# Kernel tuning notes

Hardware: AMD Instinct MI355X
Metric: run time of the kernel (lower is better)

Reference implementation:

```python
import jax, jax.numpy as jnp
import numpy as np
from jax import lax

V, E, H = 32000, 512, 512
B, K, S, T = 16, 8, 50, 40
SOS, EOS, UNK, PAD = 2, 3, 0, 1
MIN_LEN, DD, NEG = 3, 0.1, -1e20
N = B * K


def setup_inputs():
    key = jax.random.key(0)
    ks = jax.random.split(key, 12)
    w = lambda k, sh: jax.random.normal(k, sh, dtype=jnp.float32) * 0.05
    return {
        "src": jax.random.randint(ks[0], (S, B), 4, V, dtype=jnp.int32),
        "src_len": jax.random.randint(ks[1], (B,), 5, S + 1, dtype=jnp.int32),
        "embed": w(ks[2], (V, E)),
        "enc_Wih": w(ks[3], (3 * H, E)), "enc_Whh": w(ks[4], (3 * H, H)),
        "enc_bih": jnp.zeros((3 * H,), jnp.float32), "enc_bhh": jnp.zeros((3 * H,), jnp.float32),
        "bridge_W": w(ks[5], (H, H)), "bridge_b": jnp.zeros((H,), jnp.float32),
        "dec_Wih": w(ks[6], (3 * H, E)), "dec_Whh": w(ks[7], (3 * H, H)),
        "dec_bih": jnp.zeros((3 * H,), jnp.float32), "dec_bhh": jnp.zeros((3 * H,), jnp.float32),
        "attn_W": w(ks[8], (H, H)),
        "comb_W": w(ks[9], (H, 2 * H)), "comb_b": jnp.zeros((H,), jnp.float32),
        "out_W": w(ks[10], (V, H)), "out_b": jnp.zeros((V,), jnp.float32),
    }


def _gru_cell(x, h, Wih, Whh, bih, bhh):
    # torch nn.GRU cell math
    gi = x @ Wih.T + bih
    gh = h @ Whh.T + bhh
    ir, iz, inn = jnp.split(gi, 3, axis=-1)
    hr, hz, hn = jnp.split(gh, 3, axis=-1)
    r = jax.nn.sigmoid(ir + hr)
    z = jax.nn.sigmoid(iz + hz)
    n = jnp.tanh(inn + r * hn)
    return (1.0 - z) * n + z * h


def _beam_search(src, src_len, embed, enc_Wih, enc_Whh, enc_bih, enc_bhh,
                 bridge_W, bridge_b, dec_Wih, dec_Whh, dec_bih, dec_bhh,
                 attn_W, comb_W, comb_b, out_W, out_b):
    # ---- encoder: uni-dir GRU with length masking ----
    def enc_step(h, xt):
        x_t, t = xt
        hn = _gru_cell(embed[x_t], h, enc_Wih, enc_Whh, enc_bih, enc_bhh)
        h = jnp.where((t < src_len)[:, None], hn, h)
        return h, h

    h_fin, enc_outs = lax.scan(enc_step, jnp.zeros((B, H), embed.dtype), (src, jnp.arange(S)))
    hidden = jnp.tanh(h_fin @ bridge_W.T + bridge_b)  # LinearBridge

    # ---- beam expansion (repeat_interleave over batch dim) ----
    enc_bank = jnp.repeat(enc_outs, K, axis=1).transpose(1, 0, 2)  # [N,S,H]
    src_len_b = jnp.repeat(src_len, K)                              # [N]
    hidden = jnp.repeat(hidden, K, axis=0)                          # [N,H]
    attn_mask = jnp.arange(S)[None, :] < src_len_b[:, None]         # [N,S]

    def dec_step(tok, h):
        h = _gru_cell(embed[tok], h, dec_Wih, dec_Whh, dec_bih, dec_bhh)
        sc = jnp.einsum('nh,nsh->ns', h @ attn_W.T, enc_bank)
        a = jax.nn.softmax(jnp.where(attn_mask, sc, -1e9), axis=-1)
        ctx = jnp.einsum('ns,nsh->nh', a, enc_bank)
        o = jnp.tanh(jnp.concatenate([h, ctx], axis=-1) @ comb_W.T + comb_b)
        return jax.nn.log_softmax(o @ out_W.T + out_b, axis=-1), h

    padding_logits = jnp.full((B, K, K), NEG, jnp.float32).at[:, :, 0].set(0.0)
    dd_off = jnp.broadcast_to(-(jnp.arange(K, dtype=jnp.float32) * DD), (B, K, K))
    flat_offsets = jnp.repeat(jnp.arange(0, N, K), K)  # [N]

    last_token = jnp.full((N,), SOS, jnp.int32)
    tokens = jnp.zeros((T, N), jnp.int32).at[0].set(last_token)
    ending = jnp.zeros((N,), bool)
    dec_len = jnp.zeros((N,), jnp.float32)
    beam_scores = jnp.zeros((T, B, K), jnp.float32).at[0].set(
        jnp.full((B, K), NEG, jnp.float32).at[:, 0].set(0.0))

    def step(carry, t):
        last_token, hidden, ending, dec_len, beam_scores, tokens = carry
        logp, hidden = dec_step(last_token, hidden)
        logp = logp.at[:, EOS].set(jnp.where(t <= MIN_LEN, NEG, logp[:, EOS]))
        logp = logp.at[:, UNK].set(NEG)  # disable_unk_output
        p = logp.reshape(B, K, V)
        tk_sc, tk_idx = lax.top_k(p, K)                       # [B,K,K]
        tk_sc = tk_sc + jnp.where(t > 1, 1.0, 0.0) * dd_off   # diverse decoding
        endf = ending.reshape(B, K, 1)
        fin = jnp.where(endf, -tk_sc + padding_logits, 0.0)   # finished-beam offsets
        total = beam_scores.sum(axis=0)                        # [B,K]
        tot = (tk_sc + total[:, :, None] + fin).reshape(B, K * K)
        cur = (tk_sc + fin).reshape(B, K * K)
        tmp_len = jnp.where(ending, dec_len, dec_len + 1.0)
        grp_tok = tk_idx.reshape(B, K * K)
        _, sel = lax.top_k(tot, K)                             # [B,K]
        sel_tok = jnp.take_along_axis(grp_tok, sel, axis=1)
        cur_sc = jnp.take_along_axis(cur, sel, axis=1)
        flat_idx = (sel // K).reshape(-1) + flat_offsets
        hidden = hidden[flat_offsets]  # faithful: source uses flatten_offsets here
        beam_scores = beam_scores.reshape(T, N)[:, flat_idx].reshape(T, B, K)
        tokens = tokens[:, flat_idx]
        ending = ending[flat_idx]
        dec_len = tmp_len[flat_idx]
        last_token = jnp.where(ending, PAD, sel_tok.reshape(-1)).astype(jnp.int32)
        tokens = tokens.at[t].set(last_token)
        beam_scores = beam_scores.at[t].set(
            cur_sc * (last_token.reshape(B, K) != PAD).astype(jnp.float32))
        ending = ending | (last_token == EOS)
        return (last_token, hidden, ending, dec_len, beam_scores, tokens), None

    carry = (last_token, hidden, ending, dec_len, beam_scores, tokens)
    (_, _, _, _, beam_scores, tokens), _ = lax.scan(step, carry, jnp.arange(1, T))
    return tokens, beam_scores.reshape(T, N)


def reference(src, src_len, embed, enc_Wih, enc_Whh, enc_bih, enc_bhh,
              bridge_W, bridge_b, dec_Wih, dec_Whh, dec_bih, dec_bhh,
              attn_W, comb_W, comb_b, out_W, out_b):
    tokens, beam_scores = _beam_search(src, src_len, embed, enc_Wih, enc_Whh,
                                       enc_bih, enc_bhh, bridge_W, bridge_b,
                                       dec_Wih, dec_Whh, dec_bih, dec_bhh,
                                       attn_W, comb_W, comb_b, out_W, out_b)
    output_probs = jnp.zeros((T, N, V), jnp.float32)  # allocated but never written, as in source
    return output_probs, tokens, beam_scores
```

## Files before the change

### kernel.cpp

```cpp
#include <hip/hip_runtime.h>

#define DEVFN __device__ __forceinline__

constexpr int V=32000, E=512, H=512, B=16, K=8, S=50, T=40, N=128;
constexpr int SOS=2, EOS=3, UNK=0, PAD=1, MIN_LEN=3;
constexpr float DD=0.1f;
constexpr float FNEG=-1e20f;

constexpr long long PROBS_ELEMS = 163840000LL;
constexpr int TOK_OUT_OFF = 163840000;
constexpr int BS_OUT_OFF  = 163845120;

constexpr int LOGITS_O = 0;
constexpr int WTOUT_O  = 4200000;
constexpr int WTEIH_O  = 20600000;
constexpr int WTEHH_O  = 21400000;
constexpr int WTDIH_O  = 22200000;
constexpr int WTDHH_O  = 23000000;
constexpr int WTATT_O  = 23800000;
constexpr int WTCMB_O  = 24100000;
constexpr int WTBRG_O  = 24700000;
constexpr int ENC_O    = 25000000;
constexpr int HST_O    = 25500000;
constexpr int HID_O    = 25520000;
constexpr int HNEW_O   = 25600000;
constexpr int CTX_O    = 25680000;
constexpr int OVEC_O   = 25760000;
constexpr int QVEC_O   = 25840000;
constexpr int TKSC_O   = 25920000;
constexpr int TKIX_O   = 25930000;
constexpr int TOK0_O   = 25940000;
constexpr int TOK1_O   = 25950000;
constexpr int BS0_O    = 25960000;
constexpr int BS1_O    = 25970000;
constexpr int END_O    = 25980000;
constexpr int LTOK_O   = 25990000;

DEVFN float sigm(float x){ return 1.0f/(1.0f + expf(-x)); }

__global__ void tr_k(const float* __restrict__ in, float* __restrict__ out, int R, int C){
  __shared__ float t[32][33];
  int bx = blockIdx.x, by = blockIdx.y;
  int x = threadIdx.x & 31, y0 = threadIdx.x >> 5;
  for (int yy = y0; yy < 32; yy += 8){
    t[yy][x] = in[(long long)(by*32+yy)*C + bx*32 + x];
  }
  __syncthreads();
  for (int yy = y0; yy < 32; yy += 8){
    out[(long long)(bx*32+yy)*R + by*32 + x] = t[x][yy];
  }
}

__global__ void init_k(float* sc){
  int idx = blockIdx.x*256 + threadIdx.x;
  int* tok0 = (int*)(sc + TOK0_O);
  float* bs0 = sc + BS0_O;
  if (idx < T*N){
    tok0[idx] = (idx < N) ? SOS : 0;
    bs0[idx]  = (idx < N && (idx & 7)) ? FNEG : 0.0f;
  }
  if (idx < N){
    ((int*)(sc + END_O))[idx] = 0;
    ((int*)(sc + LTOK_O))[idx] = SOS;
  }
  if (idx < 2*B*H) sc[HST_O + idx] = 0.0f;
}

__global__ void zero_k(float4* __restrict__ p){
  long long idx = (long long)blockIdx.x*256 + threadIdx.x;
  long long stride = (long long)gridDim.x*256;
  const long long n4 = PROBS_ELEMS/4;
  float4 z; z.x=0.f; z.y=0.f; z.z=0.f; z.w=0.f;
  for (long long u = idx; u < n4; u += stride) p[u] = z;
}

__global__ __launch_bounds__(384) void enc2_k(const int* __restrict__ src, const int* __restrict__ srclen,
    const float* __restrict__ embed, const float* __restrict__ wtih, const float* __restrict__ wthh,
    const float* __restrict__ bih, const float* __restrict__ bhh, float* sc, int t){
  int ic = blockIdx.x;
  int b  = blockIdx.y;
  int tid = threadIdx.x;
  int p = tid >> 6;
  int il = tid & 63;
  int i = ic*64 + il;
  __shared__ __align__(16) float e[512];
  __shared__ __align__(16) float h[512];
  __shared__ float gsh[6][64];
  const float* hsrc = sc + HST_O + (t&1)*B*H + b*H;
  float* hdst = sc + HST_O + ((t&1)^1)*B*H + b*H;
  int tok = src[t*B + b];
  for (int u = tid; u < 512; u += 384){
    e[u] = embed[(long long)tok*E + u];
    h[u] = hsrc[u];
  }
  __syncthreads();
  float acc = 0.0f;
  if (p < 3){
    const float* w = wtih + p*512 + i;
    for (int k=0;k<512;k++) acc += e[k]*w[(long long)k*1536];
  } else {
    const float* w = wthh + (p-3)*512 + i;
    for (int k=0;k<512;k++) acc += h[k]*w[(long long)k*1536];
  }
  gsh[p][il] = acc;
  __syncthreads();
  if (tid < 64){
    int ii = ic*64 + tid;
    float r = sigm(gsh[0][tid] + bih[ii] + gsh[3][tid] + bhh[ii]);
    float z = sigm(gsh[1][tid] + bih[512+ii] + gsh[4][tid] + bhh[512+ii]);
    float nn = tanhf(gsh[2][tid] + bih[1024+ii] + r*(gsh[5][tid] + bhh[1024+ii]));
    float hnew = (1.0f - z)*nn + z*h[ii];
    float hout = (t < srclen[b]) ? hnew : h[ii];
    hdst[ii] = hout;
    sc[ENC_O + ((long long)t*B + b)*H + ii] = hout;
  }
}

__global__ __launch_bounds__(256) void bridge_k(const float* __restrict__ wtb, const float* __restrict__ bb, float* sc){
  int b = blockIdx.x; int tid = threadIdx.x;
  __shared__ __align__(16) float hf[512];
  const float* hsrc = sc + HST_O + (S&1)*B*H + b*H;
  ((float2*)hf)[tid] = ((const float2*)hsrc)[tid];
  __syncthreads();
  for (int ii=0; ii<2; ii++){
    int i = tid + ii*256;
    float acc = bb[i];
    for (int k=0;k<512;k++) acc += hf[k]*wtb[(long long)k*512 + i];
    float hb = tanhf(acc);
    for (int q=0;q<K;q++) sc[HID_O + ((long long)(b*K+q))*H + i] = hb;
  }
}

__global__ __launch_bounds__(256) void grudec_k(const float* __restrict__ embed,
     const float* __restrict__ wtih, const float* __restrict__ wthh,
     const float* __restrict__ bih, const float* __restrict__ bhh, float* sc){
  int il = threadIdx.x & 63, n = threadIdx.x >> 6;
  int i = blockIdx.x*64 + il;
  int nb = blockIdx.y*4;
  __shared__ __align__(16) float e4[4][512];
  __shared__ __align__(16) float hp4[4][512];
  const int* ltok = (const int*)(sc + LTOK_O);
  for (int u = threadIdx.x; u < 4*128; u += 256){
    int r = u >> 7, c = u & 127;
    ((float4*)e4[r])[c]  = ((const float4*)(embed + (long long)ltok[nb+r]*E))[c];
    ((float4*)hp4[r])[c] = ((const float4*)(sc + HID_O + (long long)(nb+r)*H))[c];
  }
  __syncthreads();
  float ar=0,az=0,an=0,hr=0,hz=0,hn=0;
  for (int k=0;k<512;k++){
    const float* wi = wtih + (long long)k*1536;
    const float* wh = wthh + (long long)k*1536;
    float wr=wi[i], wz=wi[512+i], wn=wi[1024+i];
    float ur=wh[i], uz=wh[512+i], un=wh[1024+i];
    float e0=e4[n][k], p0=hp4[n][k];
    ar+=e0*wr; az+=e0*wz; an+=e0*wn; hr+=p0*ur; hz+=p0*uz; hn+=p0*un;
  }
  float br=bih[i], bz=bih[512+i], bn=bih[1024+i];
  float cr=bhh[i], cz=bhh[512+i], cn=bhh[1024+i];
  float r = sigm(ar+br+hr+cr);
  float z = sigm(az+bz+hz+cz);
  float nn = tanhf(an+bn + r*(hn+cn));
  sc[HNEW_O + (long long)(nb+n)*H + i] = (1.0f-z)*nn + z*hp4[n][i];
}

__global__ __launch_bounds__(256) void qgemm_k(const float* __restrict__ wta, float* sc){
  int il = threadIdx.x & 63, n = threadIdx.x >> 6;
  int i = blockIdx.x*64 + il;
  int nb = blockIdx.y*4;
  __shared__ __align__(16) float hn4[4][512];
  for (int u = threadIdx.x; u < 4*128; u += 256){
    int r = u>>7, c = u&127;
    ((float4*)hn4[r])[c] = ((const float4*)(sc + HNEW_O + (long long)(nb+r)*H))[c];
  }
  __syncthreads();
  float a0=0;
  for (int k=0;k<512;k++){
    float w = wta[(long long)k*512 + i];
    a0 += hn4[n][k]*w;
  }
  sc[QVEC_O + (long long)(nb+n)*H + i] = a0;
}

__global__ __launch_bounds__(256) void att_k(const int* __restrict__ srclen, float* sc){
  int n = blockIdx.x; int g = n >> 3;
  int tid = threadIdx.x, lane = tid & 63, wave = tid >> 6;
  __shared__ __align__(16) float ql[512];
  __shared__ float al[64];
  if (tid < 128) ((float4*)ql)[tid] = ((const float4*)(sc + QVEC_O + (long long)n*H))[tid];
  __syncthreads();
  const float* enc = sc + ENC_O;
  for (int s = wave; s < S; s += 4){
    const float* er = enc + ((long long)s*B + g)*H;
    float p = 0;
    #pragma unroll
    for (int j=0;j<8;j++) p += ql[lane + 64*j]*er[lane + 64*j];
    #pragma unroll
    for (int off=32; off; off>>=1) p += __shfl_xor(p, off, 64);
    if (lane==0) al[s] = p;
  }
  __syncthreads();
  if (wave==0){
    int len = srclen[g];
    float v = (lane < S && lane < len) ? al[lane] : -1e9f;
    float m = v;
    #pragma unroll
    for (int off=32; off; off>>=1) m = fmaxf(m, __shfl_xor(m, off, 64));
    float ee = (lane < S) ? expf(v - m) : 0.0f;
    float ssum = ee;
    #pragma unroll
    for (int off=32; off; off>>=1) ssum += __shfl_xor(ssum, off, 64);
    if (lane < S) al[lane] = ee/ssum;
  }
  __syncthreads();
  for (int ii=0; ii<2; ii++){
    int i = tid + ii*256;
    float acc = 0;
    for (int s=0;s<S;s++) acc += al[s]*enc[((long long)s*B+g)*H + i];
    sc[CTX_O + (long long)n*H + i] = acc;
  }
}

__global__ __launch_bounds__(256) void comb_k(const float* __restrict__ wtc, const float* __restrict__ cb, float* sc){
  int il = threadIdx.x & 63, n = threadIdx.x >> 6;
  int i = blockIdx.x*64 + il;
  int nb = blockIdx.y*4;
  __shared__ __align__(16) float hn4[4][512];
  __shared__ __align__(16) float cx4[4][512];
  for (int u = threadIdx.x; u < 4*128; u += 256){
    int r = u>>7, c = u&127;
    ((float4*)hn4[r])[c] = ((const float4*)(sc + HNEW_O + (long long)(nb+r)*H))[c];
    ((float4*)cx4[r])[c] = ((const float4*)(sc + CTX_O + (long long)(nb+r)*H))[c];
  }
  __syncthreads();
  float a0=cb[i];
  for (int k=0;k<512;k++){
    float w = wtc[(long long)k*512 + i];
    a0 += hn4[n][k]*w;
  }
  for (int k=0;k<512;k++){
    float w = wtc[(long long)(512+k)*512 + i];
    a0 += cx4[n][k]*w;
  }
  sc[OVEC_O + (long long)(nb+n)*H + i] = tanhf(a0);
}

__global__ __launch_bounds__(256) void logits_k(const float* __restrict__ wto, const float* __restrict__ ob, float* sc){
  int v = blockIdx.x*1024 + threadIdx.x*4;
  int nb = blockIdx.y*16;
  __shared__ __align__(16) float o16[16][512];
  for (int u = threadIdx.x; u < 16*128; u += 256){
    int r = u>>7, c = u&127;
    ((float4*)o16[r])[c] = ((const float4*)(sc + OVEC_O + (long long)(nb + r)*H))[c];
  }
  __syncthreads();
  if (v >= V) return;
  float acc[16][4] = {};
  const float* wp = wto + v;
  float4 c0 = *((const float4*)(wp));
  float4 c1 = *((const float4*)(wp + V));
  float4 c2 = *((const float4*)(wp + 2LL*V));
  float4 c3 = *((const float4*)(wp + 3LL*V));
  for (int k=0;k<512;k+=4){
    float4 n0v=c0, n1v=c1, n2v=c2, n3v=c3;
    if (k < 508){
      const float* np_ = wp + (long long)(k+4)*V;
      n0v = *((const float4*)(np_));
      n1v = *((const float4*)(np_ + V));
      n2v = *((const float4*)(np_ + 2LL*V));
      n3v = *((const float4*)(np_ + 3LL*V));
    }
    #pragma unroll
    for (int j=0;j<16;j++){
      float4 o = *((const float4*)&o16[j][k]);
      acc[j][0] += o.x*c0.x + o.y*c1.x + o.z*c2.x + o.w*c3.x;
      acc[j][1] += o.x*c0.y + o.y*c1.y + o.z*c2.y + o.w*c3.y;
      acc[j][2] += o.x*c0.z + o.y*c1.z + o.z*c2.z + o.w*c3.z;
      acc[j][3] += o.x*c0.w + o.y*c1.w + o.z*c2.w + o.w*c3.w;
    }
    c0=n0v; c1=n1v; c2=n2v; c3=n3v;
  }
  float4 bbv = *((const float4*)(ob + v));
  #pragma unroll
  for (int j=0;j<16;j++){
    float4 r;
    r.x = acc[j][0]+bbv.x; r.y = acc[j][1]+bbv.y; r.z = acc[j][2]+bbv.z; r.w = acc[j][3]+bbv.w;
    *((float4*)(sc + LOGITS_O + (long long)(nb+j)*V + v)) = r;
  }
}

__global__ __launch_bounds__(256) void topk_k(float* sc, int t){
  int n = blockIdx.x, tid = threadIdx.x;
  const float4* row4 = (const float4*)(sc + LOGITS_O + (long long)n*V);
  __shared__ float rv[256];
  __shared__ float mv[256][8];
  __shared__ int   mi[256][8];
  float lm = -INFINITY;
  for (int u = tid; u < V/4; u += 256){
    float4 x = row4[u];
    lm = fmaxf(lm, fmaxf(fmaxf(x.x,x.y), fmaxf(x.z,x.w)));
  }
  rv[tid] = lm; __syncthreads();
  for (int s2=128; s2; s2>>=1){ if (tid<s2) rv[tid]=fmaxf(rv[tid],rv[tid+s2]); __syncthreads(); }
  float rmax = rv[0]; __syncthreads();
  float tv[8]; int ti[8];
  #pragma unroll
  for (int j=0;j<8;j++){ tv[j] = -INFINITY; ti[j] = V; }
  float ls = 0;
  for (int u = tid; u < V/4; u += 256){
    float4 x = row4[u];
    ls += expf(x.x-rmax)+expf(x.y-rmax)+expf(x.z-rmax)+expf(x.w-rmax);
    #pragma unroll
    for (int c=0;c<4;c++){
      int idx = u*4+c;
      float val = (c==0)?x.x:(c==1)?x.y:(c==2)?x.z:x.w;
      bool masked = (idx==UNK) || (idx==EOS && t<=MIN_LEN);
      if (!masked && val > tv[7]){
        tv[7] = val; ti[7] = idx;
        #pragma unroll
        for (int j=7;j>0;j--){
          if (tv[j] > tv[j-1]){
            float tf=tv[j]; tv[j]=tv[j-1]; tv[j-1]=tf;
            int tii=ti[j]; ti[j]=ti[j-1]; ti[j-1]=tii;
          }
        }
      }
    }
  }
  rv[tid] = ls;
  #pragma unroll
  for (int j=0;j<8;j++){ mv[tid][j]=tv[j]; mi[tid][j]=ti[j]; }
  __syncthreads();
  for (int s2=128; s2; s2>>=1){ if (tid<s2) rv[tid]+=rv[tid+s2]; __syncthreads(); }
  float lsum = logf(rv[0]);
  for (int s2=128; s2; s2>>=1){
    if (tid < s2){
      float ra[8]; int ri_[8];
      int pa=0, pb=0;
      #pragma unroll
      for (int o=0;o<8;o++){
        float va = mv[tid][pa<8?pa:7];   int xa = mi[tid][pa<8?pa:7];
        float vb = mv[tid+s2][pb<8?pb:7]; int xb = mi[tid+s2][pb<8?pb:7];
        bool ava = (pa<8), avb = (pb<8);
        bool ta;
        if (!ava) ta = false;
        else if (!avb) ta = true;
        else ta = (va > vb) || (va == vb && xa < xb);
        ra[o] = ta ? va : vb; ri_[o] = ta ? xa : xb;
        pa += ta ? 1 : 0; pb += ta ? 0 : 1;
      }
      #pragma unroll
      for (int o=0;o<8;o++){ mv[tid][o]=ra[o]; mi[tid][o]=ri_[o]; }
    }
    __syncthreads();
  }
  if (tid < 8){
    sc[TKSC_O + n*8 + tid] = (mv[0][tid] - rmax) - lsum;
    ((int*)(sc + TKIX_O))[n*8 + tid] = mi[0][tid];
  }
}

__global__ __launch_bounds__(64) void beam_k(float* sc, int t){
  int b = blockIdx.x, lane = threadIdx.x;
  const float* tksc = sc + TKSC_O;
  const int* tkix = (const int*)(sc + TKIX_O);
  int* endp = (int*)(sc + END_O);
  int* ltok = (int*)(sc + LTOK_O);
  const int* tokc; int* tokn; const float* bsc; float* bsn;
  if (t & 1){ tokc=(const int*)(sc+TOK0_O); tokn=(int*)(sc+TOK1_O); bsc=sc+BS0_O; bsn=sc+BS1_O; }
  else      { tokc=(const int*)(sc+TOK1_O); tokn=(int*)(sc+TOK0_O); bsc=sc+BS1_O; bsn=sc+BS0_O; }
  __shared__ int selp[8]; __shared__ int newtok[8]; __shared__ float newsc[8]; __shared__ int newend[8];
  if (lane == 0){
    float tot[64]; float cur[64]; int tix[64];
    for (int k=0;k<8;k++){
      float tp = 0;
      for (int u=0;u<T;u++) tp += bsc[u*N + b*8 + k];
      int ek = endp[b*8+k];
      for (int j=0;j<8;j++){
        float scv = tksc[(b*8+k)*8 + j];
        if (t > 1) scv -= DD * (float)j;
        float fin = ek ? (-scv + (j==0 ? 0.0f : FNEG)) : 0.0f;
        tot[k*8+j] = (scv + tp) + fin;
        cur[k*8+j] = scv + fin;
        tix[k*8+j] = tkix[(b*8+k)*8 + j];
      }
    }
    for (int q=0;q<8;q++){
      int best = 0; float bv = tot[0];
      for (int c=1;c<64;c++){
        if (tot[c] > bv){ bv = tot[c]; best = c; }
      }
      int p = best >> 3;
      int en = endp[b*8+p];
      int tk2 = tix[best];
      int lt = en ? PAD : tk2;
      selp[q] = p;
      newtok[q] = lt;
      newsc[q] = (lt != PAD) ? cur[best] : 0.0f;
      newend[q] = (en || lt == EOS) ? 1 : 0;
      tot[best] = -INFINITY;
    }
  }
  __syncthreads();
  for (int u = lane; u < T*8; u += 64){
    int tp2 = u >> 3, jp = u & 7;
    int p = selp[jp];
    tokn[tp2*N + b*8 + jp] = tokc[tp2*N + b*8 + p];
    bsn[tp2*N + b*8 + jp]  = bsc[tp2*N + b*8 + p];
  }
  __syncthreads();
  if (lane < 8){
    tokn[t*N + b*8 + lane] = newtok[lane];
    bsn[t*N + b*8 + lane]  = newsc[lane];
    ltok[b*8+lane] = newtok[lane];
    endp[b*8+lane] = newend[lane];
  }
  const float4* hsrc = (const float4*)(sc + HNEW_O + (long long)(b*8)*H);
  float4* hdst = (float4*)(sc + HID_O + (long long)(b*8)*H);
  for (int u = lane; u < 8*128; u += 64){
    int jp = u >> 7, c = u & 127;
    hdst[jp*128 + c] = hsrc[c];
  }
}

__global__ void emit_k(float* out, float* sc){
  int idx = blockIdx.x*256 + threadIdx.x;
  if (idx < T*N){
    out[TOK_OUT_OFF + idx] = (float)(((const int*)(sc + TOK1_O))[idx]);
    out[BS_OUT_OFF + idx]  = sc[BS1_O + idx];
  }
}

extern "C" void kernel_launch(void* const* d_in, const int* in_sizes, int n_in,
                              void* d_out, int out_size, void* d_ws, size_t ws_size,
                              hipStream_t stream){
  const int*   src    = (const int*)d_in[0];
  const int*   srclen = (const int*)d_in[1];
  const float* embed  = (const float*)d_in[2];
  const float* eWih   = (const float*)d_in[3];
  const float* eWhh   = (const float*)d_in[4];
  const float* ebih   = (const float*)d_in[5];
  const float* ebhh   = (const float*)d_in[6];
  const float* brW    = (const float*)d_in[7];
  const float* brb    = (const float*)d_in[8];
  const float* dWih   = (const float*)d_in[9];
  const float* dWhh   = (const float*)d_in[10];
  const float* dbih   = (const float*)d_in[11];
  const float* dbhh   = (const float*)d_in[12];
  const float* attW   = (const float*)d_in[13];
  const float* cmbW   = (const float*)d_in[14];
  const float* cmbb   = (const float*)d_in[15];
  const float* outW   = (const float*)d_in[16];
  const float* outb   = (const float*)d_in[17];
  float* sc = (float*)d_out;

  tr_k<<<dim3(16,48),256,0,stream>>>(eWih, sc+WTEIH_O, 1536, 512);
  tr_k<<<dim3(16,48),256,0,stream>>>(eWhh, sc+WTEHH_O, 1536, 512);
  tr_k<<<dim3(16,48),256,0,stream>>>(dWih, sc+WTDIH_O, 1536, 512);
  tr_k<<<dim3(16,48),256,0,stream>>>(dWhh, sc+WTDHH_O, 1536, 512);
  tr_k<<<dim3(16,16),256,0,stream>>>(attW, sc+WTATT_O, 512, 512);
  tr_k<<<dim3(32,16),256,0,stream>>>(cmbW, sc+WTCMB_O, 512, 1024);
  tr_k<<<dim3(16,16),256,0,stream>>>(brW,  sc+WTBRG_O, 512, 512);
  tr_k<<<dim3(16,1000),256,0,stream>>>(outW, sc+WTOUT_O, 32000, 512);
  init_k<<<64,256,0,stream>>>(sc);

  for (int t=0; t<S; t++)
    enc2_k<<<dim3(8,16),384,0,stream>>>(src, srclen, embed, sc+WTEIH_O, sc+WTEHH_O, ebih, ebhh, sc, t);
  bridge_k<<<16,256,0,stream>>>(sc+WTBRG_O, brb, sc);

  for (int t=1; t<T; t++){
    grudec_k<<<dim3(8,32),256,0,stream>>>(embed, sc+WTDIH_O, sc+WTDHH_O, dbih, dbhh, sc);
    qgemm_k<<<dim3(8,32),256,0,stream>>>(sc+WTATT_O, sc);
    att_k<<<128,256,0,stream>>>(srclen, sc);
    comb_k<<<dim3(8,32),256,0,stream>>>(sc+WTCMB_O, cmbb, sc);
    logits_k<<<dim3(32,8),256,0,stream>>>(sc+WTOUT_O, outb, sc);
    topk_k<<<128,256,0,stream>>>(sc, t);
    beam_k<<<16,64,0,stream>>>(sc, t);
  }

  emit_k<<<20,256,0,stream>>>((float*)d_out, sc);
  zero_k<<<2048,256,0,stream>>>((float4*)d_out);
}
```

Baseline: 12.18 ms.

## Split attention context and top-k over two blocks per beam row

The attention kernel now runs two blocks per row, each computing half of the context vector. Each block still recomputes the scores and softmax, so that work is duplicated. The top-k kernel is split into two partial blocks per row over halves of the vocabulary. Each writes its partial top-8, max and exp-sum to a scratch area, and beam_k merges the two halves with a log-sum-exp combine. This raises block count from 128 to 256 to fill more compute units, at the cost of duplicated score work and an extra merge step.

Result: faster. 11.62 ms (-4.6%).

```diff
diff --git a/kernel.cpp b/kernel.cpp
--- a/kernel.cpp
+++ b/kernel.cpp
@@ -35,6 +35,7 @@
 constexpr int BS1_O    = 25970000;
 constexpr int END_O    = 25980000;
 constexpr int LTOK_O   = 25990000;
+constexpr int PART_O   = 26000000;
 
 DEVFN float sigm(float x){ return 1.0f/(1.0f + expf(-x)); }
 
@@ -182,7 +183,8 @@
 }
 
 __global__ __launch_bounds__(256) void att_k(const int* __restrict__ srclen, float* sc){
-  int n = blockIdx.x; int g = n >> 3;
+  int hc = blockIdx.x;
+  int n = blockIdx.y; int g = n >> 3;
   int tid = threadIdx.x, lane = tid & 63, wave = tid >> 6;
   __shared__ __align__(16) float ql[512];
   __shared__ float al[64];
@@ -212,8 +214,8 @@
     if (lane < S) al[lane] = ee/ssum;
   }
   __syncthreads();
-  for (int ii=0; ii<2; ii++){
-    int i = tid + ii*256;
+  {
+    int i = hc*256 + tid;
     float acc = 0;
     for (int s=0;s<S;s++) acc += al[s]*enc[((long long)s*B+g)*H + i];
     sc[CTX_O + (long long)n*H + i] = acc;
@@ -288,14 +290,15 @@
   }
 }
 
-__global__ __launch_bounds__(256) void topk_k(float* sc, int t){
-  int n = blockIdx.x, tid = threadIdx.x;
+__global__ __launch_bounds__(256) void topkp_k(float* sc, int t){
+  int hc = blockIdx.x, n = blockIdx.y, tid = threadIdx.x;
   const float4* row4 = (const float4*)(sc + LOGITS_O + (long long)n*V);
+  const int u0 = hc*4000, u1 = u0 + 4000;
   __shared__ float rv[256];
   __shared__ float mv[256][8];
   __shared__ int   mi[256][8];
   float lm = -INFINITY;
-  for (int u = tid; u < V/4; u += 256){
+  for (int u = u0 + tid; u < u1; u += 256){
     float4 x = row4[u];
     lm = fmaxf(lm, fmaxf(fmaxf(x.x,x.y), fmaxf(x.z,x.w)));
   }
@@ -306,7 +309,7 @@
   #pragma unroll
   for (int j=0;j<8;j++){ tv[j] = -INFINITY; ti[j] = V; }
   float ls = 0;
-  for (int u = tid; u < V/4; u += 256){
+  for (int u = u0 + tid; u < u1; u += 256){
     float4 x = row4[u];
     ls += expf(x.x-rmax)+expf(x.y-rmax)+expf(x.z-rmax)+expf(x.w-rmax);
     #pragma unroll
@@ -331,7 +334,6 @@
   for (int j=0;j<8;j++){ mv[tid][j]=tv[j]; mi[tid][j]=ti[j]; }
   __syncthreads();
   for (int s2=128; s2; s2>>=1){ if (tid<s2) rv[tid]+=rv[tid+s2]; __syncthreads(); }
-  float lsum = logf(rv[0]);
   for (int s2=128; s2; s2>>=1){
     if (tid < s2){
       float ra[8]; int ri_[8];
@@ -353,22 +355,42 @@
     }
     __syncthreads();
   }
-  if (tid < 8){
-    sc[TKSC_O + n*8 + tid] = (mv[0][tid] - rmax) - lsum;
-    ((int*)(sc + TKIX_O))[n*8 + tid] = mi[0][tid];
+  if (tid == 0){
+    float* pp = sc + PART_O + ((long long)n*2 + hc)*20;
+    #pragma unroll
+    for (int o=0;o<8;o++){ pp[o] = mv[0][o]; ((int*)pp)[8+o] = mi[0][o]; }
+    pp[16] = rmax; pp[17] = rv[0];
   }
 }
 
 __global__ __launch_bounds__(64) void beam_k(float* sc, int t){
   int b = blockIdx.x, lane = threadIdx.x;
-  const float* tksc = sc + TKSC_O;
-  const int* tkix = (const int*)(sc + TKIX_O);
   int* endp = (int*)(sc + END_O);
   int* ltok = (int*)(sc + LTOK_O);
   const int* tokc; int* tokn; const float* bsc; float* bsn;
   if (t & 1){ tokc=(const int*)(sc+TOK0_O); tokn=(int*)(sc+TOK1_O); bsc=sc+BS0_O; bsn=sc+BS1_O; }
   else      { tokc=(const int*)(sc+TOK1_O); tokn=(int*)(sc+TOK0_O); bsc=sc+BS1_O; bsn=sc+BS0_O; }
+  __shared__ float tks[64]; __shared__ int tki[64];
   __shared__ int selp[8]; __shared__ int newtok[8]; __shared__ float newsc[8]; __shared__ int newend[8];
+  if (lane < 8){
+    const float* pA = sc + PART_O + ((long long)(b*8+lane)*2 + 0)*20;
+    const float* pB = pA + 20;
+    float mA = pA[16], mB = pB[16];
+    float gm = fmaxf(mA, mB);
+    float ss = pA[17]*expf(mA-gm) + pB[17]*expf(mB-gm);
+    float lsum = logf(ss);
+    int pa=0, pb=0;
+    for (int o=0;o<8;o++){
+      int ia = pa<8?pa:7, ib = pb<8?pb:7;
+      float va = pA[ia]; int xa = ((const int*)pA)[8+ia];
+      float vb = pB[ib]; int xb = ((const int*)pB)[8+ib];
+      bool ta = (pa<8) && ((pb>=8) || (va > vb) || (va == vb && xa < xb));
+      tks[lane*8+o] = ((ta?va:vb) - gm) - lsum;
+      tki[lane*8+o] = ta?xa:xb;
+      pa += ta?1:0; pb += ta?0:1;
+    }
+  }
+  __syncthreads();
   if (lane == 0){
     float tot[64]; float cur[64]; int tix[64];
     for (int k=0;k<8;k++){
@@ -376,12 +398,12 @@
       for (int u=0;u<T;u++) tp += bsc[u*N + b*8 + k];
       int ek = endp[b*8+k];
       for (int j=0;j<8;j++){
-        float scv = tksc[(b*8+k)*8 + j];
+        float scv = tks[k*8 + j];
         if (t > 1) scv -= DD * (float)j;
         float fin = ek ? (-scv + (j==0 ? 0.0f : FNEG)) : 0.0f;
         tot[k*8+j] = (scv + tp) + fin;
         cur[k*8+j] = scv + fin;
-        tix[k*8+j] = tkix[(b*8+k)*8 + j];
+        tix[k*8+j] = tki[k*8 + j];
       }
     }
     for (int q=0;q<8;q++){
@@ -470,10 +492,10 @@
   for (int t=1; t<T; t++){
     grudec_k<<<dim3(8,32),256,0,stream>>>(embed, sc+WTDIH_O, sc+WTDHH_O, dbih, dbhh, sc);
     qgemm_k<<<dim3(8,32),256,0,stream>>>(sc+WTATT_O, sc);
-    att_k<<<128,256,0,stream>>>(srclen, sc);
+    att_k<<<dim3(2,128),256,0,stream>>>(srclen, sc);
     comb_k<<<dim3(8,32),256,0,stream>>>(sc+WTCMB_O, cmbb, sc);
     logits_k<<<dim3(32,8),256,0,stream>>>(sc+WTOUT_O, outb, sc);
-    topk_k<<<128,256,0,stream>>>(sc, t);
+    topkp_k<<<dim3(2,128),256,0,stream>>>(sc, t);
     beam_k<<<16,64,0,stream>>>(sc, t);
   }
 
```
